# Performance work log

Measured on AMD Instinct MI355X. Metric: run time of the kernel, lower is better.

## Reference

```python
import jax, jax.numpy as jnp
import numpy as np

D = 1024
H = 16
K = D // H
B = 2
S = 2048

def setup_inputs() -> dict:
    key = jax.random.key(0)
    k1, k2, k3, k4, k5 = jax.random.split(key, 5)
    x = jax.random.normal(k1, (B, S, D), dtype=jnp.float32)
    # nn.Linear(d, 3d): weight [3d, d], bias [3d]
    Wqkv = jax.random.normal(k2, (3 * D, D), dtype=jnp.float32) / np.sqrt(D)
    bqkv = jax.random.normal(k3, (3 * D,), dtype=jnp.float32) * 0.01
    Wproj = jax.random.normal(k4, (D, D), dtype=jnp.float32) / np.sqrt(D)
    bproj = jax.random.normal(k5, (D,), dtype=jnp.float32) * 0.01
    return {"x": x, "Wqkv": Wqkv, "bqkv": bqkv, "Wproj": Wproj, "bproj": bproj}

def reference(x, Wqkv, bqkv, Wproj, bproj):
    Bsz, Slen, d = x.shape
    # fused QKV projection: [B,S,3d] -> [B,S,3,H,K] -> (3, B, H, S, K)
    qkv = (jnp.einsum('bsd,ed->bse', x, Wqkv) + bqkv).reshape(Bsz, Slen, 3, H, K)
    q, k, v = jnp.moveaxis(qkv, 2, 0).transpose(0, 1, 3, 2, 4)
    scale = 1.0 / jnp.sqrt(jnp.asarray(K, dtype=x.dtype))
    scores = jnp.einsum('bhqk,bhmk->bhqm', q, k) * scale  # [B,H,S,S]
    a = jax.nn.softmax(scores, axis=-1)
    # dropout is identity in eval mode
    o = jnp.einsum('bhqm,bhmk->bhqk', a, v)  # [B,H,S,K]
    o = o.transpose(0, 2, 1, 3).reshape(Bsz, Slen, d)
    return jnp.einsum('bsd,ed->bse', o, Wproj) + bproj
```

## Files before the change

### kernel.cpp

```cpp
#include <hip/hip_runtime.h>
#include <cstdint>

typedef unsigned short ushort_t;
typedef short short8 __attribute__((ext_vector_type(8)));
typedef float f32x4 __attribute__((ext_vector_type(4)));
typedef float float4v __attribute__((ext_vector_type(4)));
typedef unsigned int uint2v __attribute__((ext_vector_type(2)));

#define DDIM 1024
#define HH 16
#define HEADK 64
#define BB 2
#define SS 2048

#if __has_builtin(__builtin_amdgcn_exp2f)
#define EXP2F(x) __builtin_amdgcn_exp2f(x)
#else
#define EXP2F(x) exp2f(x)
#endif

__device__ __forceinline__ ushort_t f2bf(float f) {
  union { float f; uint32_t u; } c; c.f = f;
  uint32_t u = c.u;
  u += 0x7fffu + ((u >> 16) & 1u);
  return (ushort_t)(u >> 16);
}

__device__ __forceinline__ uint32_t pkbf_trunc(float a, float b) {
  union { float f; uint32_t u; } ca, cb;
  ca.f = a; cb.f = b;
  return __builtin_amdgcn_perm(cb.u, ca.u, 0x07060302);
}

__device__ __forceinline__ uint32_t pkbf_rne(float a, float b) {
  return (uint32_t)f2bf(a) | ((uint32_t)f2bf(b) << 16);
}

__device__ __forceinline__ float bfhi2f(uint32_t u) {
  union { uint32_t u; float f; } c; c.u = u & 0xffff0000u; return c.f;
}
__device__ __forceinline__ float bflo2f(uint32_t u) {
  union { uint32_t u; float f; } c; c.u = u << 16; return c.f;
}

__device__ __forceinline__ void glds16(const ushort_t* gp, ushort_t* lp) {
  __builtin_amdgcn_global_load_lds(
      (const __attribute__((address_space(1))) uint32_t*)gp,
      (__attribute__((address_space(3))) uint32_t*)lp, 16, 0, 0);
}

__global__ void cvt3_kernel(const float* __restrict__ s0, ushort_t* __restrict__ d0, int n0,
                            const float* __restrict__ s1, ushort_t* __restrict__ d1, int n1,
                            const float* __restrict__ s2, ushort_t* __restrict__ d2, int n2) {
  int i = blockIdx.x * blockDim.x + threadIdx.x;
  const float* src; ushort_t* dst; int k;
  if (i < n0) { src = s0; dst = d0; k = i; }
  else if (i < n0 + n1) { src = s1; dst = d1; k = i - n0; }
  else if (i < n0 + n1 + n2) { src = s2; dst = d2; k = i - n0 - n1; }
  else return;
  float4v v = ((const float4v*)src)[k];
  uint2v o; o[0] = pkbf_rne(v[0], v[1]); o[1] = pkbf_rne(v[2], v[3]);
  ((uint2v*)dst)[k] = o;
}

__global__ __launch_bounds__(512, 2) void gemm_qkv(
    const ushort_t* __restrict__ A, const ushort_t* __restrict__ Bm,
    const float* __restrict__ bias, ushort_t* __restrict__ Cbf) {
  constexpr int Kd = 1024;
  __shared__ ushort_t smem[65536];
  const int tid = threadIdx.x;
  const int wv = tid >> 6, lane = tid & 63;
  const int l15 = lane & 15, quad = lane >> 4;
  const int wm = wv >> 2, wn = wv & 3;
  const int tm0 = blockIdx.y * 256, tn0 = blockIdx.x * 256;
  const int lrow = lane >> 3;
  const int gcb = (lane & 7) ^ lrow;

  f32x4 acc[8][4];
#pragma unroll
  for (int i = 0; i < 8; ++i)
#pragma unroll
    for (int j = 0; j < 4; ++j) acc[i][j] = (f32x4){0.f, 0.f, 0.f, 0.f};

  auto stage = [&](int t, int buf) {
    ushort_t* As = smem + buf * 32768;
    ushort_t* Bs = As + 16384;
    const int k0 = t * 64;
#pragma unroll
    for (int c = 0; c < 4; ++c) {
      int seg = wv * 4 + c;
      glds16(A + (size_t)(tm0 + seg * 8 + lrow) * Kd + k0 + gcb * 8,
             As + seg * 512);
      glds16(Bm + (size_t)(tn0 + seg * 8 + lrow) * Kd + k0 + gcb * 8,
             Bs + seg * 512);
    }
  };

  stage(0, 0);
  for (int t = 0; t < 16; ++t) {
    const int cur = t & 1;
    asm volatile("" ::: "memory");
    __builtin_amdgcn_s_barrier();
    if (t + 1 < 16) {
      stage(t + 1, cur ^ 1);
      asm volatile("s_waitcnt vmcnt(8)" ::: "memory");
    } else {
      asm volatile("s_waitcnt vmcnt(0)" ::: "memory");
    }
    __builtin_amdgcn_s_barrier();
    asm volatile("" ::: "memory");
    __builtin_amdgcn_sched_barrier(0);

    const ushort_t* As = smem + cur * 32768;
    const ushort_t* Bs = As + 16384;
    short8 bfr[4][2];
#pragma unroll
    for (int j = 0; j < 4; ++j)
#pragma unroll
      for (int kc = 0; kc < 2; ++kc) {
        int n = wn * 64 + j * 16 + l15;
        bfr[j][kc] =
            *(const short8*)(Bs + n * 64 + (((kc * 4 + quad) ^ (l15 & 7)) << 3));
      }
#pragma unroll
    for (int q = 0; q < 4; ++q) {
      short8 af[2][2];
#pragma unroll
      for (int i2 = 0; i2 < 2; ++i2)
#pragma unroll
        for (int kc = 0; kc < 2; ++kc) {
          int r = wm * 128 + (q * 2 + i2) * 16 + l15;
          af[i2][kc] =
              *(const short8*)(As + r * 64 + (((kc * 4 + quad) ^ (l15 & 7)) << 3));
        }
      __builtin_amdgcn_s_setprio(1);
#pragma unroll
      for (int kc = 0; kc < 2; ++kc)
#pragma unroll
        for (int i2 = 0; i2 < 2; ++i2)
#pragma unroll
          for (int j = 0; j < 4; ++j)
            acc[q * 2 + i2][j] = __builtin_amdgcn_mfma_f32_16x16x32_bf16(
                af[i2][kc], bfr[j][kc], acc[q * 2 + i2][j], 0, 0, 0);
      __builtin_amdgcn_s_setprio(0);
    }
  }

  const int tsel = tn0 >> 10;
  if (tsel < 2) {
#pragma unroll
    for (int j = 0; j < 4; ++j) {
      int col = tn0 + wn * 64 + j * 16 + l15;
      float bv = bias[col];
      int hh = (col >> 6) & 15, kk2 = col & 63;
#pragma unroll
      for (int mi = 0; mi < 8; ++mi) {
        int row0 = tm0 + wm * 128 + mi * 16 + quad * 4;
#pragma unroll
        for (int r = 0; r < 4; ++r) {
          int row = row0 + r;
          int b = row >> 11, s = row & 2047;
          float v = acc[mi][j][r] + bv;
          if (tsel == 0) v *= 0.18033688f;
          size_t base = (((size_t)tsel * BB + b) * HH + hh) * ((size_t)SS * HEADK);
          Cbf[base + (size_t)s * HEADK + kk2] = f2bf(v);
        }
      }
    }
  } else {
    __builtin_amdgcn_s_barrier();
    ushort_t* slab = smem + wv * 8192;
#pragma unroll
    for (int j = 0; j < 4; ++j) {
      int c = j * 16 + l15;
      float bv = bias[tn0 + wn * 64 + c];
#pragma unroll
      for (int mi = 0; mi < 8; ++mi) {
        int row0 = mi * 16 + quad * 4;
        uint2v dw;
        dw[0] = pkbf_rne(acc[mi][j][0] + bv, acc[mi][j][1] + bv);
        dw[1] = pkbf_rne(acc[mi][j][2] + bv, acc[mi][j][3] + bv);
        int rb = row0 >> 3;
        *(uint2v*)(&slab[c * 128 + (((rb ^ (c & 15)) << 3) | (row0 & 7))]) = dw;
      }
    }
    const int r2 = lane & 15, cg = lane >> 4;
#pragma unroll
    for (int it = 0; it < 16; ++it) {
      int c = it * 4 + cg;
      short8 vv = *(const short8*)(&slab[c * 128 + ((r2 ^ (c & 15)) << 3)]);
      int gcol = tn0 + wn * 64 + c;
      int hh = (gcol >> 6) & 15, kk2 = gcol & 63;
      int grow = tm0 + wm * 128 + r2 * 8;
      int b = grow >> 11, s = grow & 2047;
      size_t base = (((size_t)2 * BB + b) * HH + hh) * ((size_t)SS * HEADK);
      *(short8*)(&Cbf[base + (size_t)kk2 * SS + s]) = vv;
    }
  }
}

template <int MODE, int TM>
__global__ __launch_bounds__(256) void gemm_nt(
    const ushort_t* __restrict__ A, const ushort_t* __restrict__ Bm,
    const float* __restrict__ bias, float* __restrict__ Cout,
    ushort_t* __restrict__ Cbf, int M, int N, int Kd) {
  __shared__ ushort_t smem[128 * 64 * 2];
  ushort_t* As = smem;
  ushort_t* Bs = smem + TM * 64;
  const int MI = TM / 32;
  const int tid = threadIdx.x;
  const int wv = tid >> 6, lane = tid & 63;
  const int l15 = lane & 15, quad = lane >> 4;
  const int wm = wv >> 1, wn = wv & 1;
  const int tm0 = blockIdx.y * TM, tn0 = blockIdx.x * 128;

  f32x4 acc[MI][4];
#pragma unroll
  for (int i = 0; i < MI; ++i)
#pragma unroll
    for (int j = 0; j < 4; ++j) acc[i][j] = (f32x4){0.f, 0.f, 0.f, 0.f};

  const int lrow = lane >> 3;
  const int gcb = (lane & 7) ^ lrow;
  const int ACI = TM / 32;

  for (int k0 = 0; k0 < Kd; k0 += 64) {
#pragma unroll
    for (int c = 0; c < ACI; ++c) {
      int seg = wv * ACI + c;
      glds16(A + (size_t)(tm0 + seg * 8 + lrow) * Kd + k0 + gcb * 8,
             As + seg * 512);
    }
#pragma unroll
    for (int c = 0; c < 4; ++c) {
      int seg = wv * 4 + c;
      glds16(Bm + (size_t)(tn0 + seg * 8 + lrow) * Kd + k0 + gcb * 8,
             Bs + seg * 512);
    }
    __syncthreads();
#pragma unroll
    for (int kk = 0; kk < 64; kk += 32) {
      short8 af[MI], bfr[4];
#pragma unroll
      for (int i = 0; i < MI; ++i) {
        int r = wm * (TM / 2) + i * 16 + l15;
        int cb = (kk >> 3) + quad;
        af[i] = *(const short8*)(As + r * 64 + ((cb ^ (l15 & 7)) << 3));
      }
#pragma unroll
      for (int j = 0; j < 4; ++j) {
        int r = wn * 64 + j * 16 + l15;
        int cb = (kk >> 3) + quad;
        bfr[j] = *(const short8*)(Bs + r * 64 + ((cb ^ (l15 & 7)) << 3));
      }
#pragma unroll
      for (int i = 0; i < MI; ++i)
#pragma unroll
        for (int j = 0; j < 4; ++j)
          acc[i][j] = __builtin_amdgcn_mfma_f32_16x16x32_bf16(
              af[i], bfr[j], acc[i][j], 0, 0, 0);
    }
    __syncthreads();
  }

  if (MODE == 1) {
#pragma unroll
    for (int j = 0; j < 4; ++j) {
      int col = tn0 + wn * 64 + j * 16 + l15;
      float bv = bias[col];
#pragma unroll
      for (int i = 0; i < MI; ++i) {
        int row0 = tm0 + wm * (TM / 2) + i * 16 + quad * 4;
#pragma unroll
        for (int r = 0; r < 4; ++r)
          Cout[(size_t)(row0 + r) * N + col] = acc[i][j][r] + bv;
      }
    }
  }
}

template <int NSPLIT>
__global__ __launch_bounds__(256, 4) void attn_kernel(
    const ushort_t* __restrict__ qkv, ushort_t* __restrict__ O0,
    ushort_t* __restrict__ O1, float* __restrict__ Lp) {
  constexpr int NT = (SS / NSPLIT) / 32;
  __shared__ ushort_t Kt[3][32 * 64];
  __shared__ ushort_t Vt[3][64 * 32];
  __shared__ ushort_t Pw[4][2][32 * 32];

  const int qt = blockIdx.x, h = blockIdx.y;
  const int b = blockIdx.z / NSPLIT, ns = blockIdx.z % NSPLIT;
  const int tid = threadIdx.x;
  const int wv = tid >> 6, lane = tid & 63;
  const int l15 = lane & 15, quad = lane >> 4;

  const size_t hstride = (size_t)SS * HEADK;
  const ushort_t* Qg = qkv + ((size_t)(0 * BB + b) * HH + h) * hstride;
  const ushort_t* Kg = qkv + ((size_t)(1 * BB + b) * HH + h) * hstride;
  const ushort_t* Vg = qkv + ((size_t)(2 * BB + b) * HH + h) * hstride;
  ushort_t* Opp = ns ? O1 : O0;

  short8 qf[2][2];
#pragma unroll
  for (int mi = 0; mi < 2; ++mi)
#pragma unroll
    for (int kc = 0; kc < 2; ++kc)
      qf[mi][kc] = *(const short8*)(
          Qg + (size_t)(qt * 128 + wv * 32 + mi * 16 + l15) * 64 + kc * 32 +
          quad * 8);

  const short ONE = (short)0x3F80;
  short8 ones = {ONE, ONE, ONE, ONE, ONE, ONE, ONE, ONE};

  f32x4 oat[2][4];
  f32x4 loa[2];
#pragma unroll
  for (int mi = 0; mi < 2; ++mi) {
    loa[mi] = (f32x4){0.f, 0.f, 0.f, 0.f};
#pragma unroll
    for (int c = 0; c < 4; ++c) oat[mi][c] = (f32x4){0.f, 0.f, 0.f, 0.f};
  }

  const int lrow = lane >> 3, gcb = (lane & 7) ^ lrow;
  const int vfl = lane >> 2;
  const int vgb = (lane & 3) ^ ((vfl >> 1) & 3);

  const int pos0 = ns * (SS / NSPLIT);

  auto stage = [&](int jj, int db) {
    glds16(Kg + (size_t)(pos0 + jj * 32 + wv * 8 + lrow) * 64 + gcb * 8,
           &Kt[db][wv * 512]);
    glds16(Vg + (size_t)(wv * 16 + vfl) * SS + pos0 + jj * 32 + vgb * 8,
           &Vt[db][wv * 512]);
  };

  auto qk_phase = [&](int kb, int pb) {
    f32x4 st[2][2];
    __builtin_amdgcn_s_setprio(1);
#pragma unroll
    for (int cf = 0; cf < 2; ++cf) {
      int n = cf * 16 + l15;
      short8 kf0 = *(const short8*)(&Kt[kb][n * 64 + ((quad ^ (n & 7)) << 3)]);
      short8 kf1 =
          *(const short8*)(&Kt[kb][n * 64 + (((quad + 4) ^ (n & 7)) << 3)]);
#pragma unroll
      for (int mi = 0; mi < 2; ++mi) {
        f32x4 z = (f32x4){0.f, 0.f, 0.f, 0.f};
        z = __builtin_amdgcn_mfma_f32_16x16x32_bf16(kf0, qf[mi][0], z, 0, 0, 0);
        z = __builtin_amdgcn_mfma_f32_16x16x32_bf16(kf1, qf[mi][1], z, 0, 0, 0);
        st[mi][cf] = z;
      }
    }
    __builtin_amdgcn_s_setprio(0);
#pragma unroll
    for (int mi = 0; mi < 2; ++mi)
#pragma unroll
      for (int cf = 0; cf < 2; ++cf) {
        float e0 = EXP2F(st[mi][cf][0]);
        float e1 = EXP2F(st[mi][cf][1]);
        float e2 = EXP2F(st[mi][cf][2]);
        float e3 = EXP2F(st[mi][cf][3]);
        uint2v dw;
        dw[0] = pkbf_trunc(e0, e1);
        dw[1] = pkbf_trunc(e2, e3);
        int row = mi * 16 + l15;
        int pbv = 2 * cf + (quad >> 1);
        int pbs = pbv ^ ((l15 >> 1) & 3);
        *(uint2v*)(&Pw[wv][pb][row * 32 + pbs * 8 + (quad & 1) * 4]) = dw;
      }
  };

  stage(0, 0);
  stage(1, 1);

  asm volatile("s_waitcnt vmcnt(2)" ::: "memory");
  __builtin_amdgcn_s_barrier();
  asm volatile("" ::: "memory");
  __builtin_amdgcn_sched_barrier(0);
  qk_phase(0, 0);

  int vb = 0;
  for (int j = 0; j < NT; ++j) {
    const int kb = (vb == 2) ? 0 : vb + 1;
    const int sb = (kb == 2) ? 0 : kb + 1;
    asm volatile("s_waitcnt vmcnt(0)" ::: "memory");
    __builtin_amdgcn_s_barrier();
    asm volatile("" ::: "memory");
    __builtin_amdgcn_sched_barrier(0);

    if (j + 2 < NT) stage(j + 2, sb);
    if (j + 1 < NT) qk_phase(kb, (j + 1) & 1);

    short8 pa[2];
#pragma unroll
    for (int mi = 0; mi < 2; ++mi) {
      int row = mi * 16 + l15;
      pa[mi] = *(const short8*)(&Pw[wv][j & 1][row * 32 +
                                              ((quad ^ ((l15 >> 1) & 3)) << 3)]);
    }
    __builtin_amdgcn_s_setprio(1);
#pragma unroll
    for (int cf = 0; cf < 4; ++cf) {
      short8 vf = *(const short8*)(&Vt[vb][(cf * 16 + l15) * 32 +
                                           ((quad ^ ((l15 >> 1) & 3)) << 3)]);
#pragma unroll
      for (int mi = 0; mi < 2; ++mi)
        oat[mi][cf] = __builtin_amdgcn_mfma_f32_16x16x32_bf16(
            vf, pa[mi], oat[mi][cf], 0, 0, 0);
    }
#pragma unroll
    for (int mi = 0; mi < 2; ++mi)
      loa[mi] = __builtin_amdgcn_mfma_f32_16x16x32_bf16(ones, pa[mi], loa[mi],
                                                        0, 0, 0);
    __builtin_amdgcn_s_setprio(0);

    vb = kb;
  }

  const size_t obase = ((size_t)b * HH + h) * SS * HEADK;
#pragma unroll
  for (int mi = 0; mi < 2; ++mi) {
#pragma unroll
    for (int cf = 0; cf < 4; ++cf) {
      uint2v dw;
      dw[0] = pkbf_rne(oat[mi][cf][0], oat[mi][cf][1]);
      dw[1] = pkbf_rne(oat[mi][cf][2], oat[mi][cf][3]);
      int cb = 2 * cf + (quad >> 1);
      int cbs = cb ^ (l15 & 7);
      *(uint2v*)(&Pw[wv][0][l15 * 64 + cbs * 8 + (quad & 1) * 4]) = dw;
    }
    const int r = lane >> 2;
#pragma unroll
    for (int pass = 0; pass < 2; ++pass) {
      int g = (lane & 3) + 4 * pass;
      short8 ov = *(const short8*)(&Pw[wv][0][r * 64 + ((g ^ (r & 7)) << 3)]);
      int qrow = qt * 128 + wv * 32 + mi * 16 + r;
      *(short8*)(&Opp[obase + (size_t)qrow * 64 + g * 8]) = ov;
    }
    if (quad == 0) {
      int qrow = qt * 128 + wv * 32 + mi * 16 + l15;
      Lp[((size_t)(ns * BB + b) * HH + h) * SS + qrow] = loa[mi][0];
    }
  }
}

template <int NSPLIT>
__global__ void reduce_kernel(const ushort_t* __restrict__ O0,
                              const ushort_t* __restrict__ O1,
                              const float* __restrict__ Lp,
                              ushort_t* __restrict__ ob) {
  const size_t nsL = (size_t)BB * HH * SS;
  int c = blockIdx.x * blockDim.x + threadIdx.x;
  int fc = c & 7;
  int hh = (c >> 3) & 15;
  int row = c >> 7;
  int b = row >> 11, s = row & 2047;
  size_t po = (((size_t)b * HH + hh) * SS + s) * 64 + fc * 8;
  size_t lo = ((size_t)b * HH + hh) * SS + s;
  const ushort_t* Ops[2] = {O0, O1};
  float acc[8];
#pragma unroll
  for (int i = 0; i < 8; ++i) acc[i] = 0.f;
  float l = 0.f;
#pragma unroll
  for (int t = 0; t < NSPLIT; ++t) {
    uint2v a0 = *(const uint2v*)(&Ops[t][po]);
    uint2v a1 = *(const uint2v*)(&Ops[t][po + 4]);
    acc[0] += bflo2f(a0[0]); acc[1] += bfhi2f(a0[0]);
    acc[2] += bflo2f(a0[1]); acc[3] += bfhi2f(a0[1]);
    acc[4] += bflo2f(a1[0]); acc[5] += bfhi2f(a1[0]);
    acc[6] += bflo2f(a1[1]); acc[7] += bfhi2f(a1[1]);
    l += Lp[(size_t)t * nsL + lo];
  }
  float inv = 1.0f / l;
  uint2v o0, o1;
  o0[0] = pkbf_rne(acc[0] * inv, acc[1] * inv);
  o0[1] = pkbf_rne(acc[2] * inv, acc[3] * inv);
  o1[0] = pkbf_rne(acc[4] * inv, acc[5] * inv);
  o1[1] = pkbf_rne(acc[6] * inv, acc[7] * inv);
  size_t oo = ((size_t)(b * SS + s)) * DDIM + hh * 64 + fc * 8;
  *(uint2v*)(&ob[oo]) = o0;
  *(uint2v*)(&ob[oo + 4]) = o1;
}

extern "C" void kernel_launch(void* const* d_in, const int* in_sizes, int n_in,
                              void* d_out, int out_size, void* d_ws,
                              size_t ws_size, hipStream_t stream) {
  const float* x = (const float*)d_in[0];
  const float* Wqkv = (const float*)d_in[1];
  const float* bqkv = (const float*)d_in[2];
  const float* Wproj = (const float*)d_in[3];
  const float* bproj = (const float*)d_in[4];
  float* out = (float*)d_out;

  ushort_t* xb = (ushort_t*)d_ws;
  ushort_t* wqb = xb + (size_t)4096 * 1024;
  ushort_t* wpb = wqb + (size_t)3072 * 1024;
  ushort_t* qkvb = wpb + (size_t)1024 * 1024;
  ushort_t* Op1 = qkvb + (size_t)3 * BB * HH * SS * HEADK;
  ushort_t* Op0 = xb;
  float* Lp = (float*)wqb;
  ushort_t* obuf = qkvb;

  const int n0 = 4096 * 1024 / 4, n1 = 3072 * 1024 / 4, n2 = 1024 * 1024 / 4;
  cvt3_kernel<<<(n0 + n1 + n2 + 255) / 256, 256, 0, stream>>>(
      x, xb, n0, Wqkv, wqb, n1, Wproj, wpb, n2);
  gemm_qkv<<<dim3(3072 / 256, 4096 / 256), 512, 0, stream>>>(xb, wqb, bqkv,
                                                             qkvb);
  attn_kernel<2><<<dim3(16, 16, BB * 2), 256, 0, stream>>>(qkvb, Op0, Op1, Lp);
  reduce_kernel<2><<<(BB * SS * DDIM / 8) / 256, 256, 0, stream>>>(Op0, Op1,
                                                                   Lp, obuf);
  gemm_nt<1, 64><<<dim3(1024 / 128, 4096 / 64), 256, 0, stream>>>(
      obuf, wpb, bproj, out, nullptr, 4096, 1024, 1024);
}
```

Baseline: 186.0 us.

## Fuse split-KV reduction into output projection GEMM and remap attention blocks per XCD

```diff
diff --git a/kernel.cpp b/kernel.cpp
--- a/kernel.cpp
+++ b/kernel.cpp
@@ -6,6 +6,7 @@
 typedef float f32x4 __attribute__((ext_vector_type(4)));
 typedef float float4v __attribute__((ext_vector_type(4)));
 typedef unsigned int uint2v __attribute__((ext_vector_type(2)));
+typedef unsigned int uint4v __attribute__((ext_vector_type(4)));
 
 #define DDIM 1024
 #define HH 16
@@ -199,82 +200,135 @@
   }
 }
 
-template <int MODE, int TM>
-__global__ __launch_bounds__(256) void gemm_nt(
-    const ushort_t* __restrict__ A, const ushort_t* __restrict__ Bm,
-    const float* __restrict__ bias, float* __restrict__ Cout,
-    ushort_t* __restrict__ Cbf, int M, int N, int Kd) {
-  __shared__ ushort_t smem[128 * 64 * 2];
-  ushort_t* As = smem;
-  ushort_t* Bs = smem + TM * 64;
-  const int MI = TM / 32;
+__global__ __launch_bounds__(512, 2) void gemm_proj(
+    const ushort_t* __restrict__ Op0, const ushort_t* __restrict__ Op1,
+    const float* __restrict__ Lp, const ushort_t* __restrict__ Bm,
+    const float* __restrict__ bias, float* __restrict__ Cout) {
+  constexpr int Kd = 1024;
+  constexpr size_t nsL = (size_t)BB * HH * SS;
+  __shared__ ushort_t smem[32768];
   const int tid = threadIdx.x;
   const int wv = tid >> 6, lane = tid & 63;
   const int l15 = lane & 15, quad = lane >> 4;
-  const int wm = wv >> 1, wn = wv & 1;
-  const int tm0 = blockIdx.y * TM, tn0 = blockIdx.x * 128;
-
-  f32x4 acc[MI][4];
-#pragma unroll
-  for (int i = 0; i < MI; ++i)
-#pragma unroll
-    for (int j = 0; j < 4; ++j) acc[i][j] = (f32x4){0.f, 0.f, 0.f, 0.f};
-
-  const int lrow = lane >> 3;
-  const int gcb = (lane & 7) ^ lrow;
-  const int ACI = TM / 32;
-
-  for (int k0 = 0; k0 < Kd; k0 += 64) {
-#pragma unroll
-    for (int c = 0; c < ACI; ++c) {
-      int seg = wv * ACI + c;
-      glds16(A + (size_t)(tm0 + seg * 8 + lrow) * Kd + k0 + gcb * 8,
-             As + seg * 512);
-    }
-#pragma unroll
-    for (int c = 0; c < 4; ++c) {
-      int seg = wv * 4 + c;
-      glds16(Bm + (size_t)(tn0 + seg * 8 + lrow) * Kd + k0 + gcb * 8,
+  const int wm = wv >> 2, wn = wv & 3;
+  const int tm0 = blockIdx.y * 128, tn0 = blockIdx.x * 128;
+  const int lrow = lane >> 3, gcb = (lane & 7) ^ lrow;
+
+  const int ar = tid >> 2, acg = tid & 3;
+  const int grow = tm0 + ar;
+  const int ab = grow >> 11, as_ = grow & 2047;
+
+  f32x4 acc[4][2];
+#pragma unroll
+  for (int i = 0; i < 4; ++i)
+#pragma unroll
+    for (int j = 0; j < 2; ++j) acc[i][j] = (f32x4){0.f, 0.f, 0.f, 0.f};
+
+  uint4v ra0, ra1, rb0, rb1;
+  float rl0, rl1;
+
+  auto readA = [&](int t) {
+    size_t lo = (size_t)(ab * HH + t) * SS + as_;
+    size_t po = lo * 64 + acg * 16;
+    ra0 = *(const uint4v*)(Op0 + po);
+    ra1 = *(const uint4v*)(Op0 + po + 8);
+    rb0 = *(const uint4v*)(Op1 + po);
+    rb1 = *(const uint4v*)(Op1 + po + 8);
+    rl0 = Lp[lo];
+    rl1 = Lp[nsL + lo];
+  };
+  auto writeA = [&](int p) {
+    float inv = 1.0f / (rl0 + rl1);
+    uint4v olo, ohi;
+#pragma unroll
+    for (int d = 0; d < 4; ++d) {
+      olo[d] = pkbf_rne((bflo2f(ra0[d]) + bflo2f(rb0[d])) * inv,
+                        (bfhi2f(ra0[d]) + bfhi2f(rb0[d])) * inv);
+      ohi[d] = pkbf_rne((bflo2f(ra1[d]) + bflo2f(rb1[d])) * inv,
+                        (bfhi2f(ra1[d]) + bfhi2f(rb1[d])) * inv);
+    }
+    ushort_t* As = smem + p * 16384;
+    *(uint4v*)(&As[ar * 64 + (((acg * 2) ^ (ar & 7)) << 3)]) = olo;
+    *(uint4v*)(&As[ar * 64 + (((acg * 2 + 1) ^ (ar & 7)) << 3)]) = ohi;
+  };
+  auto stageB = [&](int t, int p) {
+    ushort_t* Bs = smem + p * 16384 + 8192;
+#pragma unroll
+    for (int c = 0; c < 2; ++c) {
+      int seg = wv * 2 + c;
+      glds16(Bm + (size_t)(tn0 + seg * 8 + lrow) * Kd + t * 64 + gcb * 8,
              Bs + seg * 512);
     }
-    __syncthreads();
-#pragma unroll
-    for (int kk = 0; kk < 64; kk += 32) {
-      short8 af[MI], bfr[4];
-#pragma unroll
-      for (int i = 0; i < MI; ++i) {
-        int r = wm * (TM / 2) + i * 16 + l15;
-        int cb = (kk >> 3) + quad;
-        af[i] = *(const short8*)(As + r * 64 + ((cb ^ (l15 & 7)) << 3));
-      }
-#pragma unroll
-      for (int j = 0; j < 4; ++j) {
-        int r = wn * 64 + j * 16 + l15;
-        int cb = (kk >> 3) + quad;
-        bfr[j] = *(const short8*)(Bs + r * 64 + ((cb ^ (l15 & 7)) << 3));
-      }
-#pragma unroll
-      for (int i = 0; i < MI; ++i)
-#pragma unroll
-        for (int j = 0; j < 4; ++j)
-          acc[i][j] = __builtin_amdgcn_mfma_f32_16x16x32_bf16(
-              af[i], bfr[j], acc[i][j], 0, 0, 0);
-    }
-    __syncthreads();
-  }
-
-  if (MODE == 1) {
-#pragma unroll
-    for (int j = 0; j < 4; ++j) {
-      int col = tn0 + wn * 64 + j * 16 + l15;
-      float bv = bias[col];
-#pragma unroll
-      for (int i = 0; i < MI; ++i) {
-        int row0 = tm0 + wm * (TM / 2) + i * 16 + quad * 4;
-#pragma unroll
-        for (int r = 0; r < 4; ++r)
-          Cout[(size_t)(row0 + r) * N + col] = acc[i][j][r] + bv;
-      }
+  };
+
+  readA(0);
+  __builtin_amdgcn_sched_barrier(0);
+  stageB(0, 0);
+  __builtin_amdgcn_sched_barrier(0);
+  asm volatile("s_waitcnt vmcnt(2)" ::: "memory");
+  writeA(0);
+
+  for (int t = 0; t < 16; ++t) {
+    const int p = t & 1;
+    asm volatile("s_waitcnt lgkmcnt(0)" ::: "memory");
+    __builtin_amdgcn_s_barrier();
+    __builtin_amdgcn_sched_barrier(0);
+    if (t + 1 < 16) {
+      readA(t + 1);
+      __builtin_amdgcn_sched_barrier(0);
+      stageB(t + 1, p ^ 1);
+      __builtin_amdgcn_sched_barrier(0);
+      asm volatile("s_waitcnt vmcnt(8)" ::: "memory");
+    } else {
+      asm volatile("s_waitcnt vmcnt(0)" ::: "memory");
+    }
+    __builtin_amdgcn_s_barrier();
+    asm volatile("" ::: "memory");
+    __builtin_amdgcn_sched_barrier(0);
+
+    const ushort_t* As = smem + p * 16384;
+    const ushort_t* Bs = As + 8192;
+    short8 bfr[2][2], af[4][2];
+#pragma unroll
+    for (int j = 0; j < 2; ++j)
+#pragma unroll
+      for (int kc = 0; kc < 2; ++kc) {
+        int n = wn * 32 + j * 16 + l15;
+        bfr[j][kc] =
+            *(const short8*)(Bs + n * 64 + (((kc * 4 + quad) ^ (l15 & 7)) << 3));
+      }
+#pragma unroll
+    for (int mi = 0; mi < 4; ++mi)
+#pragma unroll
+      for (int kc = 0; kc < 2; ++kc) {
+        int r = wm * 64 + mi * 16 + l15;
+        af[mi][kc] =
+            *(const short8*)(As + r * 64 + (((kc * 4 + quad) ^ (l15 & 7)) << 3));
+      }
+    __builtin_amdgcn_s_setprio(1);
+#pragma unroll
+    for (int kc = 0; kc < 2; ++kc)
+#pragma unroll
+      for (int mi = 0; mi < 4; ++mi)
+#pragma unroll
+        for (int j = 0; j < 2; ++j)
+          acc[mi][j] = __builtin_amdgcn_mfma_f32_16x16x32_bf16(
+              af[mi][kc], bfr[j][kc], acc[mi][j], 0, 0, 0);
+    __builtin_amdgcn_s_setprio(0);
+
+    if (t + 1 < 16) writeA(p ^ 1);
+  }
+
+#pragma unroll
+  for (int j = 0; j < 2; ++j) {
+    int col = tn0 + wn * 32 + j * 16 + l15;
+    float bv = bias[col];
+#pragma unroll
+    for (int mi = 0; mi < 4; ++mi) {
+      int row0 = tm0 + wm * 64 + mi * 16 + quad * 4;
+#pragma unroll
+      for (int r = 0; r < 4; ++r)
+        Cout[(size_t)(row0 + r) * 1024 + col] = acc[mi][j][r] + bv;
     }
   }
 }
@@ -288,8 +342,13 @@
   __shared__ ushort_t Vt[3][64 * 32];
   __shared__ ushort_t Pw[4][2][32 * 32];
 
-  const int qt = blockIdx.x, h = blockIdx.y;
-  const int b = blockIdx.z / NSPLIT, ns = blockIdx.z % NSPLIT;
+  const int lin = blockIdx.x + 16 * (blockIdx.y + 16 * blockIdx.z);
+  const int xcd = lin & 7, ii = lin >> 3;
+  const int qt = ii & 15;
+  const int hz = (ii >> 4) * 8 + xcd;
+  const int h = hz & 15;
+  const int z = hz >> 4;
+  const int b = z >> 1, ns = z & 1;
   const int tid = threadIdx.x;
   const int wv = tid >> 6, lane = tid & 63;
   const int l15 = lane & 15, quad = lane >> 4;
@@ -345,10 +404,10 @@
           *(const short8*)(&Kt[kb][n * 64 + (((quad + 4) ^ (n & 7)) << 3)]);
 #pragma unroll
       for (int mi = 0; mi < 2; ++mi) {
-        f32x4 z = (f32x4){0.f, 0.f, 0.f, 0.f};
-        z = __builtin_amdgcn_mfma_f32_16x16x32_bf16(kf0, qf[mi][0], z, 0, 0, 0);
-        z = __builtin_amdgcn_mfma_f32_16x16x32_bf16(kf1, qf[mi][1], z, 0, 0, 0);
-        st[mi][cf] = z;
+        f32x4 z2 = (f32x4){0.f, 0.f, 0.f, 0.f};
+        z2 = __builtin_amdgcn_mfma_f32_16x16x32_bf16(kf0, qf[mi][0], z2, 0, 0, 0);
+        z2 = __builtin_amdgcn_mfma_f32_16x16x32_bf16(kf1, qf[mi][1], z2, 0, 0, 0);
+        st[mi][cf] = z2;
       }
     }
     __builtin_amdgcn_s_setprio(0);
@@ -444,45 +503,6 @@
   }
 }
 
-template <int NSPLIT>
-__global__ void reduce_kernel(const ushort_t* __restrict__ O0,
-                              const ushort_t* __restrict__ O1,
-                              const float* __restrict__ Lp,
-                              ushort_t* __restrict__ ob) {
-  const size_t nsL = (size_t)BB * HH * SS;
-  int c = blockIdx.x * blockDim.x + threadIdx.x;
-  int fc = c & 7;
-  int hh = (c >> 3) & 15;
-  int row = c >> 7;
-  int b = row >> 11, s = row & 2047;
-  size_t po = (((size_t)b * HH + hh) * SS + s) * 64 + fc * 8;
-  size_t lo = ((size_t)b * HH + hh) * SS + s;
-  const ushort_t* Ops[2] = {O0, O1};
-  float acc[8];
-#pragma unroll
-  for (int i = 0; i < 8; ++i) acc[i] = 0.f;
-  float l = 0.f;
-#pragma unroll
-  for (int t = 0; t < NSPLIT; ++t) {
-    uint2v a0 = *(const uint2v*)(&Ops[t][po]);
-    uint2v a1 = *(const uint2v*)(&Ops[t][po + 4]);
-    acc[0] += bflo2f(a0[0]); acc[1] += bfhi2f(a0[0]);
-    acc[2] += bflo2f(a0[1]); acc[3] += bfhi2f(a0[1]);
-    acc[4] += bflo2f(a1[0]); acc[5] += bfhi2f(a1[0]);
-    acc[6] += bflo2f(a1[1]); acc[7] += bfhi2f(a1[1]);
-    l += Lp[(size_t)t * nsL + lo];
-  }
-  float inv = 1.0f / l;
-  uint2v o0, o1;
-  o0[0] = pkbf_rne(acc[0] * inv, acc[1] * inv);
-  o0[1] = pkbf_rne(acc[2] * inv, acc[3] * inv);
-  o1[0] = pkbf_rne(acc[4] * inv, acc[5] * inv);
-  o1[1] = pkbf_rne(acc[6] * inv, acc[7] * inv);
-  size_t oo = ((size_t)(b * SS + s)) * DDIM + hh * 64 + fc * 8;
-  *(uint2v*)(&ob[oo]) = o0;
-  *(uint2v*)(&ob[oo + 4]) = o1;
-}
-
 extern "C" void kernel_launch(void* const* d_in, const int* in_sizes, int n_in,
                               void* d_out, int out_size, void* d_ws,
                               size_t ws_size, hipStream_t stream) {
@@ -500,16 +520,13 @@
   ushort_t* Op1 = qkvb + (size_t)3 * BB * HH * SS * HEADK;
   ushort_t* Op0 = xb;
   float* Lp = (float*)wqb;
-  ushort_t* obuf = qkvb;
 
   const int n0 = 4096 * 1024 / 4, n1 = 3072 * 1024 / 4, n2 = 1024 * 1024 / 4;
   cvt3_kernel<<<(n0 + n1 + n2 + 255) / 256, 256, 0, stream>>>(
       x, xb, n0, Wqkv, wqb, n1, Wproj, wpb, n2);
   gemm_qkv<<<dim3(3072 / 256, 4096 / 256), 512, 0, stream>>>(xb, wqb, bqkv,
                                                              qkvb);
-  attn_kernel<2><<<dim3(16, 16, BB * 2), 256, 0, stream>>>(qkvb, Op0, Op1, Lp);
-  reduce_kernel<2><<<(BB * SS * DDIM / 8) / 256, 256, 0, stream>>>(Op0, Op1,
-                                                                   Lp, obuf);
-  gemm_nt<1, 64><<<dim3(1024 / 128, 4096 / 64), 256, 0, stream>>>(
-      obuf, wpb, bproj, out, nullptr, 4096, 1024, 1024);
-}
+  attn_kernel<2><<<dim3(16, 16, 4), 256, 0, stream>>>(qkvb, Op0, Op1, Lp);
+  gemm_proj<<<dim3(1024 / 128, 4096 / 128), 512, 0, stream>>>(
+      Op0, Op1, Lp, wpb, bproj, out);
+}
```

New measurement: 186.4 us. Within noise of the previous version (+0.2%).
